# Performance work log

Measured on AMD Instinct MI355X. Metric: run time of the kernel, lower is better.

Reference implementation:

```python
import jax, jax.numpy as jnp
import numpy as np

D_MODEL = 1024
N_HEADS = 16
D_K = 64


def setup_inputs() -> dict:
    key = jax.random.key(0)
    ks = jax.random.split(key, 9)
    dkh = D_K * N_HEADS
    s = 1.0 / np.sqrt(D_MODEL)
    so = 1.0 / np.sqrt(dkh)
    return {
        "x": jax.random.normal(ks[0], (2, 2048, D_MODEL), dtype=jnp.float32),
        "Wq": jax.random.normal(ks[1], (D_MODEL, dkh), dtype=jnp.float32) * s,
        "bq": jnp.zeros((dkh,), dtype=jnp.float32),
        "Wk": jax.random.normal(ks[2], (D_MODEL, dkh), dtype=jnp.float32) * s,
        "bk": jnp.zeros((dkh,), dtype=jnp.float32),
        "Wv": jax.random.normal(ks[3], (D_MODEL, dkh), dtype=jnp.float32) * s,
        "bv": jnp.zeros((dkh,), dtype=jnp.float32),
        "Wo": jax.random.normal(ks[4], (dkh, D_MODEL), dtype=jnp.float32) * so,
        "bo": jnp.zeros((D_MODEL,), dtype=jnp.float32),
    }


def reference(x, Wq, bq, Wk, bk, Wv, bv, Wo, bo):
    B, S, _ = x.shape
    # project and split heads: [B, S, H, Dk] -> [B, H, S, Dk]
    def split(t):
        return t.reshape(B, S, N_HEADS, D_K).transpose(0, 2, 1, 3)
    q = split(x @ Wq + bq)
    k = split(x @ Wk + bk)
    v = split(x @ Wv + bv)
    scores = jnp.einsum("bhsd,bhtd->bhst", q, k) / jnp.sqrt(jnp.float32(D_K))
    weights = jax.nn.softmax(scores, axis=-1)
    out = jnp.einsum("bhst,bhtd->bhsd", weights, v)  # [B, H, S, Dk]
    out = out.transpose(0, 2, 1, 3).reshape(B, S, N_HEADS * D_K)
    return out @ Wo + bo
```

## Files before the change

kernel.cpp:

```cpp
#include <hip/hip_runtime.h>
#include <hip/hip_bf16.h>

typedef unsigned short u16;
typedef unsigned int u32;
typedef short bf16x4 __attribute__((ext_vector_type(4)));
typedef short bf16x8 __attribute__((ext_vector_type(8)));
typedef float f32x4 __attribute__((ext_vector_type(4)));
typedef u32 u32x2 __attribute__((ext_vector_type(2)));
typedef u32 u32x4 __attribute__((ext_vector_type(4)));

#define DEVINL __device__ __forceinline__

DEVINL u16 f2bf(float f) {
    u32 u = __builtin_bit_cast(u32, f);
    u32 r = u + 0x7fffu + ((u >> 16) & 1u);
    return (u16)(r >> 16);
}

DEVINL u32 pack2(float a, float b) {
    u16 lo = __builtin_bit_cast(u16, __float2bfloat16(a));
    u16 hi = __builtin_bit_cast(u16, __float2bfloat16(b));
    return (u32)lo | ((u32)hi << 16);
}

__global__ __launch_bounds__(256) void cast_x_kernel(const float4* __restrict__ in,
                                                     u16* __restrict__ outp) {
    int i = blockIdx.x * 256 + threadIdx.x;
    float4 v = in[i];
    ushort4 o;
    o.x = f2bf(v.x); o.y = f2bf(v.y); o.z = f2bf(v.z); o.w = f2bf(v.w);
    *(ushort4*)&outp[(size_t)i * 4] = o;
}

__global__ __launch_bounds__(256) void transpose_cast(
    const float* __restrict__ W0, const float* __restrict__ W1,
    const float* __restrict__ W2, const float* __restrict__ W3,
    u16* __restrict__ T0, u16* __restrict__ T1,
    u16* __restrict__ T2, u16* __restrict__ T3) {
    __shared__ __align__(16) u16 lds[64 * 68];
    int bid = blockIdx.x;
    const float* W; u16* T;
    switch (bid >> 8) {
        case 0:  W = W0; T = T0; break;
        case 1:  W = W1; T = T1; break;
        case 2:  W = W2; T = T2; break;
        default: W = W3; T = T3; break;
    }
    int tile = bid & 255;
    int k0 = (tile >> 4) << 6;
    int n0 = (tile & 15) << 6;
    int t = threadIdx.x;
    int rk = t >> 2;
    int cb = (t & 3) << 4;
#pragma unroll
    for (int j = 0; j < 4; ++j) {
        float4 v = *(const float4*)&W[(size_t)(k0 + rk) * 1024 + n0 + cb + 4 * j];
        ushort4 o;
        o.x = f2bf(v.x); o.y = f2bf(v.y); o.z = f2bf(v.z); o.w = f2bf(v.w);
        *(ushort4*)&lds[rk * 68 + cb + 4 * j] = o;
    }
    __syncthreads();
    int rn = t >> 2;
#pragma unroll
    for (int j2 = 0; j2 < 2; ++j2) {
        u16 tmp[8];
#pragma unroll
        for (int u = 0; u < 8; ++u)
            tmp[u] = lds[(cb + 8 * j2 + u) * 68 + rn];
        *(uint4*)&T[(size_t)(n0 + rn) * 1024 + k0 + cb + 8 * j2] = *(uint4*)tmp;
    }
}

template <int MODE>
__global__ __launch_bounds__(256) void gemm_kernel(
    const u16* __restrict__ A,
    const u16* __restrict__ W0t, const u16* __restrict__ W1t, const u16* __restrict__ W2t,
    const float* __restrict__ b0, const float* __restrict__ b1, const float* __restrict__ b2,
    u16* __restrict__ Oq, u16* __restrict__ Ok, u16* __restrict__ Ov,
    float* __restrict__ Fout) {
    constexpr int NB = (MODE == 0) ? 24 : 8;
    const int mb = blockIdx.x / NB, nb = blockIdx.x % NB;
    const int m0 = mb * 128, n0 = nb * 128;
    const int tid = threadIdx.x, lane = tid & 63, w = tid >> 6;
    const int wr = w >> 1, wc = w & 1;
    const int c = lane & 15, g = lane >> 4;

    __shared__ __align__(16) u16 Alds[128 * 64];
    __shared__ __align__(16) u16 Blds[128 * 64];

    const u16* Wt; const float* bias; int ncol0;
    if (MODE == 0) {
        const int tsel = n0 >> 10;
        Wt   = (tsel == 0) ? W0t : ((tsel == 1) ? W1t : W2t);
        bias = (tsel == 0) ? b0  : ((tsel == 1) ? b1  : b2);
        ncol0 = n0 & 1023;
    } else {
        Wt = W0t; bias = b0; ncol0 = n0;
    }

    const u16* Asrc = A  + (size_t)(m0    + 32 * w + (lane >> 3)) * 1024 + (lane & 7) * 8;
    const u16* Bsrc = Wt + (size_t)(ncol0 + 32 * w + (lane >> 3)) * 1024 + (lane & 7) * 8;
    u16* AldsW = &Alds[(32 * w) * 64];
    u16* BldsW = &Blds[(32 * w) * 64];

    f32x4 acc[4][4] = {};

    for (int kt = 0; kt < 16; ++kt) {
        const int k0 = kt * 64;
#pragma unroll
        for (int i = 0; i < 4; ++i) {
            __builtin_amdgcn_global_load_lds(
                (const __attribute__((address_space(1))) void*)(Asrc + k0 + i * 8 * 1024),
                (__attribute__((address_space(3))) void*)(AldsW + i * 8 * 64), 16, 0, 0);
            __builtin_amdgcn_global_load_lds(
                (const __attribute__((address_space(1))) void*)(Bsrc + k0 + i * 8 * 1024),
                (__attribute__((address_space(3))) void*)(BldsW + i * 8 * 64), 16, 0, 0);
        }
        __syncthreads();
#pragma unroll
        for (int kk = 0; kk < 2; ++kk) {
            bf16x8 af[4], bfr[4];
#pragma unroll
            for (int mf = 0; mf < 4; ++mf)
                af[mf] = *(const bf16x8*)&Alds[(c + 16 * mf + 64 * wr) * 64 + 8 * g + 32 * kk];
#pragma unroll
            for (int nf = 0; nf < 4; ++nf)
                bfr[nf] = *(const bf16x8*)&Blds[(c + 16 * nf + 64 * wc) * 64 + 8 * g + 32 * kk];
#pragma unroll
            for (int mf = 0; mf < 4; ++mf)
#pragma unroll
                for (int nf = 0; nf < 4; ++nf)
                    acc[mf][nf] = __builtin_amdgcn_mfma_f32_16x16x32_bf16(
                        af[mf], bfr[nf], acc[mf][nf], 0, 0, 0);
        }
        __syncthreads();
    }

    float biasv[4];
#pragma unroll
    for (int nf = 0; nf < 4; ++nf) biasv[nf] = bias[ncol0 + 64 * wc + 16 * nf + c];

    if (MODE == 0) {
        const int bi = m0 >> 11;
        const int tsel = n0 >> 10;
        if (tsel < 2) {
            u16* Odst = (tsel == 0) ? Oq : Ok;
            const float sc = (tsel == 0) ? 0.18033688011112042f : 1.0f;
#pragma unroll
            for (int nf = 0; nf < 4; ++nf) {
                const int n_in = ncol0 + 64 * wc + 16 * nf + c;
                const int h = n_in >> 6, d = n_in & 63;
                u16* base = Odst + ((size_t)(bi * 16 + h)) * 2048 * 64 + d;
#pragma unroll
                for (int mf = 0; mf < 4; ++mf)
#pragma unroll
                    for (int r = 0; r < 4; ++r) {
                        const int m = m0 + 64 * wr + 16 * mf + 4 * g + r;
                        const int s = m & 2047;
                        base[(size_t)s * 64] = f2bf((acc[mf][nf][r] + biasv[nf]) * sc);
                    }
            }
        } else {
#pragma unroll
            for (int nf = 0; nf < 4; ++nf) {
                const int n_in = ncol0 + 64 * wc + 16 * nf + c;
                const int h = n_in >> 6, d = n_in & 63;
                u16* base = Ov + ((size_t)((bi * 16 + h) * 64 + d)) * 2048;
#pragma unroll
                for (int mf = 0; mf < 4; ++mf) {
                    const int s = (m0 & 2047) + 64 * wr + 16 * mf + 4 * g;
                    const int r5 = s & 31;
                    const int pos = (s & ~63) + 32 * ((s >> 5) & 1)
                                  + ((r5 < 16) ? (2 * r5) : (2 * (r5 - 16) + 4));
                    u32x2 pr = {pack2(acc[mf][nf][0] + biasv[nf], acc[mf][nf][1] + biasv[nf]),
                                pack2(acc[mf][nf][2] + biasv[nf], acc[mf][nf][3] + biasv[nf])};
                    *(u32x2*)&base[pos] = pr;
                }
            }
        }
    } else {
#pragma unroll
        for (int mf = 0; mf < 4; ++mf)
#pragma unroll
            for (int r = 0; r < 4; ++r) {
                const int m = m0 + 64 * wr + 16 * mf + 4 * g + r;
                float* rowp = Fout + (size_t)m * 1024 + n0 + 64 * wc;
#pragma unroll
                for (int nf = 0; nf < 4; ++nf)
                    rowp[16 * nf + c] = acc[mf][nf][r] + biasv[nf];
            }
    }
}

__global__ __launch_bounds__(256) void attn_kernel(
    const u16* __restrict__ Q, const u16* __restrict__ K, const u16* __restrict__ Vp,
    u16* __restrict__ O) {
    const int bid0 = blockIdx.x;
    const int bid = (bid0 & 7) * 128 + (bid0 >> 3);
    const int qb = bid & 31, h = (bid >> 5) & 15, b = bid >> 9;
    const int tid = threadIdx.x, lane = tid & 63, w = tid >> 6;
    const int c = lane & 15, g = lane >> 4;

    __shared__ __align__(16) u16 KL[2][4096];
    __shared__ __align__(16) u16 VL[2][4096];

    const size_t hoff = ((size_t)(b * 16 + h)) * 2048 * 64;
    const u16* Qh = Q + hoff;
    const u16* Kh = K + hoff;
    const u16* Vh = Vp + hoff;

    const int q = qb * 64 + w * 16 + c;
    bf16x8 qf[2];
#pragma unroll
    for (int kk = 0; kk < 2; ++kk)
        qf[kk] = *(const bf16x8*)&Qh[(size_t)q * 64 + 8 * g + 32 * kk];

    const u16* kSrc = Kh + (size_t)(16 * w + (lane >> 2)) * 64 + 8 * (lane & 3);
    const u16* vSrc = Vh + (size_t)(16 * w + (lane >> 2)) * 2048 + 8 * (lane & 3);
    const int kdBase = (2 * w) * 512;

#define STAGE(bi_, kt_) do {                                                              \
        const u16* ks_ = kSrc + (kt_) * 4096;                                             \
        const u16* vs_ = vSrc + (kt_) * 64;                                               \
        __builtin_amdgcn_global_load_lds(                                                 \
            (const __attribute__((address_space(1))) void*)(ks_),                         \
            (__attribute__((address_space(3))) void*)(&KL[bi_][kdBase]), 16, 0, 0);       \
        __builtin_amdgcn_global_load_lds(                                                 \
            (const __attribute__((address_space(1))) void*)(ks_ + 32),                    \
            (__attribute__((address_space(3))) void*)(&KL[bi_][kdBase + 512]), 16, 0, 0); \
        __builtin_amdgcn_global_load_lds(                                                 \
            (const __attribute__((address_space(1))) void*)(vs_),                         \
            (__attribute__((address_space(3))) void*)(&VL[bi_][kdBase]), 16, 0, 0);       \
        __builtin_amdgcn_global_load_lds(                                                 \
            (const __attribute__((address_space(1))) void*)(vs_ + 32),                    \
            (__attribute__((address_space(3))) void*)(&VL[bi_][kdBase + 512]), 16, 0, 0); \
    } while (0)

    f32x4 oacc[4] = {};
    float mrun = -3.0e38f, lrun = 0.f;

    STAGE(0, 0);
    __syncthreads();

    for (int kt = 0; kt < 32; ++kt) {
        const int cur = kt & 1, nxt = cur ^ 1;
        if (kt < 31) STAGE(nxt, kt + 1);

        const u16* Kb0 = &KL[cur][0];
        const u16* Vb0 = &VL[cur][0];

        f32x4 sacc[4] = {};
#pragma unroll
        for (int T = 0; T < 4; ++T)
#pragma unroll
            for (int kk = 0; kk < 2; ++kk) {
                bf16x8 kf = *(const bf16x8*)&Kb0[(2 * T + kk) * 512 + 32 * c + 8 * g];
                sacc[T] = __builtin_amdgcn_mfma_f32_16x16x32_bf16(kf, qf[kk], sacc[T], 0, 0, 0);
            }

        float t0 = fmaxf(fmaxf(sacc[0][0], sacc[0][1]), fmaxf(sacc[0][2], sacc[0][3]));
        float t1 = fmaxf(fmaxf(sacc[1][0], sacc[1][1]), fmaxf(sacc[1][2], sacc[1][3]));
        float t2 = fmaxf(fmaxf(sacc[2][0], sacc[2][1]), fmaxf(sacc[2][2], sacc[2][3]));
        float t3 = fmaxf(fmaxf(sacc[3][0], sacc[3][1]), fmaxf(sacc[3][2], sacc[3][3]));
        float mx = fmaxf(fmaxf(t0, t1), fmaxf(t2, t3));
        mx = fmaxf(mx, __shfl_xor(mx, 16));
        mx = fmaxf(mx, __shfl_xor(mx, 32));

        if (__any(mx > mrun)) {
            const float mnew = fmaxf(mrun, mx);
            const float alpha = exp2f(mrun - mnew);
            mrun = mnew;
            lrun *= alpha;
#pragma unroll
            for (int dt = 0; dt < 4; ++dt)
#pragma unroll
                for (int r = 0; r < 4; ++r) oacc[dt][r] *= alpha;
        }

        u32 pw[4][2];
        float lsum = 0.f;
#pragma unroll
        for (int T = 0; T < 4; ++T) {
            float p0 = exp2f(sacc[T][0] - mrun);
            float p1 = exp2f(sacc[T][1] - mrun);
            float p2 = exp2f(sacc[T][2] - mrun);
            float p3 = exp2f(sacc[T][3] - mrun);
            lsum += (p0 + p1) + (p2 + p3);
            pw[T][0] = pack2(p0, p1);
            pw[T][1] = pack2(p2, p3);
        }
        lsum += __shfl_xor(lsum, 16);
        lsum += __shfl_xor(lsum, 32);
        lrun += lsum;

#pragma unroll
        for (int kb = 0; kb < 2; ++kb) {
            u32x4 ww = {pw[2 * kb][0], pw[2 * kb][1], pw[2 * kb + 1][0], pw[2 * kb + 1][1]};
            bf16x8 pf = __builtin_bit_cast(bf16x8, ww);
#pragma unroll
            for (int dt = 0; dt < 4; ++dt) {
                bf16x8 vf = *(const bf16x8*)&Vb0[(2 * dt + kb) * 512 + 32 * c + 8 * g];
                oacc[dt] = __builtin_amdgcn_mfma_f32_16x16x32_bf16(vf, pf, oacc[dt], 0, 0, 0);
            }
        }

        __syncthreads();
    }
#undef STAGE

    const float inv = 1.0f / lrun;
    const size_t obase = ((size_t)(b * 2048 + q)) * 1024 + h * 64 + 4 * g;
#pragma unroll
    for (int dt = 0; dt < 4; ++dt) {
        u32x2 pr = {pack2(oacc[dt][0] * inv, oacc[dt][1] * inv),
                    pack2(oacc[dt][2] * inv, oacc[dt][3] * inv)};
        *(u32x2*)&O[obase + 16 * dt] = pr;
    }
}

extern "C" void kernel_launch(void* const* d_in, const int* in_sizes, int n_in,
                              void* d_out, int out_size, void* d_ws, size_t ws_size,
                              hipStream_t stream) {
    const float* x  = (const float*)d_in[0];
    const float* Wq = (const float*)d_in[1];
    const float* bq = (const float*)d_in[2];
    const float* Wk = (const float*)d_in[3];
    const float* bk = (const float*)d_in[4];
    const float* Wv = (const float*)d_in[5];
    const float* bv = (const float*)d_in[6];
    const float* Wo = (const float*)d_in[7];
    const float* bo = (const float*)d_in[8];
    float* out = (float*)d_out;

    if (ws_size < (size_t)51 * 1024 * 1024) return;

    u16* ws  = (u16*)d_ws;
    u16* xb  = ws;
    u16* wqt = xb  + 4096 * 1024;
    u16* wkt = wqt + 1024 * 1024;
    u16* wvt = wkt + 1024 * 1024;
    u16* wot = wvt + 1024 * 1024;
    u16* Qb  = wot + 1024 * 1024;
    u16* Kb  = Qb + 4194304;
    u16* Vtb = Kb + 4194304;
    u16* Ob  = Vtb + 4194304;

    cast_x_kernel<<<4096, 256, 0, stream>>>((const float4*)x, xb);
    transpose_cast<<<1024, 256, 0, stream>>>(Wq, Wk, Wv, Wo, wqt, wkt, wvt, wot);
    gemm_kernel<0><<<768, 256, 0, stream>>>(xb, wqt, wkt, wvt, bq, bk, bv,
                                            Qb, Kb, Vtb, nullptr);
    attn_kernel<<<1024, 256, 0, stream>>>(Qb, Kb, Vtb, Ob);
    gemm_kernel<1><<<256, 256, 0, stream>>>(Ob, wot, nullptr, nullptr, bo, nullptr, nullptr,
                                            nullptr, nullptr, nullptr, out);
}
```

Measured before the change: 252.0 us.

## Enlarge attention query tile to 256 rows with 8 waves, two row tiles each

The attention kernel now uses 512-thread blocks covering 256 query rows, with each wave handling two 16-row query tiles that share every K/V fragment read from LDS. Each staged K/V tile is therefore reused by four times as many queries, which cuts global and LDS traffic per query, and the load work is spread across 8 waves. The softmax exponent switches from exp2f to __expf, and the Q prescale changes from 1/sqrt(64)*log2(e) to 1/8 so the two stay consistent. In exchange the grid shrinks to 256 blocks, roughly one per CU, and register pressure rises from the doubled accumulators, which may lower occupancy.

```diff
diff --git a/kernel.cpp b/kernel.cpp
--- a/kernel.cpp
+++ b/kernel.cpp
@@ -145,7 +145,7 @@
         const int tsel = n0 >> 10;
         if (tsel < 2) {
             u16* Odst = (tsel == 0) ? Oq : Ok;
-            const float sc = (tsel == 0) ? 0.18033688011112042f : 1.0f;
+            const float sc = (tsel == 0) ? 0.125f : 1.0f;
 #pragma unroll
             for (int nf = 0; nf < 4; ++nf) {
                 const int n_in = ncol0 + 64 * wc + 16 * nf + c;
@@ -192,12 +192,12 @@
     }
 }
 
-__global__ __launch_bounds__(256) void attn_kernel(
+__global__ __launch_bounds__(512) void attn_kernel(
     const u16* __restrict__ Q, const u16* __restrict__ K, const u16* __restrict__ Vp,
     u16* __restrict__ O) {
     const int bid0 = blockIdx.x;
-    const int bid = (bid0 & 7) * 128 + (bid0 >> 3);
-    const int qb = bid & 31, h = (bid >> 5) & 15, b = bid >> 9;
+    const int bid = (bid0 & 7) * 32 + (bid0 >> 3);
+    const int qb = bid & 7, h = (bid >> 3) & 15, b = bid >> 7;
     const int tid = threadIdx.x, lane = tid & 63, w = tid >> 6;
     const int c = lane & 15, g = lane >> 4;
 
@@ -209,35 +209,29 @@
     const u16* Kh = K + hoff;
     const u16* Vh = Vp + hoff;
 
-    const int q = qb * 64 + w * 16 + c;
-    bf16x8 qf[2];
-#pragma unroll
-    for (int kk = 0; kk < 2; ++kk)
-        qf[kk] = *(const bf16x8*)&Qh[(size_t)q * 64 + 8 * g + 32 * kk];
-
-    const u16* kSrc = Kh + (size_t)(16 * w + (lane >> 2)) * 64 + 8 * (lane & 3);
-    const u16* vSrc = Vh + (size_t)(16 * w + (lane >> 2)) * 2048 + 8 * (lane & 3);
-    const int kdBase = (2 * w) * 512;
+    const int q0 = qb * 256 + w * 32;
+    bf16x8 qf[2][2];
+#pragma unroll
+    for (int u = 0; u < 2; ++u)
+#pragma unroll
+        for (int kk = 0; kk < 2; ++kk)
+            qf[u][kk] = *(const bf16x8*)&Qh[(size_t)(q0 + 16 * u + c) * 64 + 8 * g + 32 * kk];
+
+    const u16* kSrc = Kh + (size_t)(16 * (w >> 1) + (lane >> 2)) * 64 + 32 * (w & 1) + 8 * (lane & 3);
+    const u16* vSrc = Vh + (size_t)(16 * (w >> 1) + (lane >> 2)) * 2048 + 32 * (w & 1) + 8 * (lane & 3);
+    const int dBase = w * 512;
 
 #define STAGE(bi_, kt_) do {                                                              \
-        const u16* ks_ = kSrc + (kt_) * 4096;                                             \
-        const u16* vs_ = vSrc + (kt_) * 64;                                               \
         __builtin_amdgcn_global_load_lds(                                                 \
-            (const __attribute__((address_space(1))) void*)(ks_),                         \
-            (__attribute__((address_space(3))) void*)(&KL[bi_][kdBase]), 16, 0, 0);       \
+            (const __attribute__((address_space(1))) void*)(kSrc + (kt_) * 4096),         \
+            (__attribute__((address_space(3))) void*)(&KL[bi_][dBase]), 16, 0, 0);        \
         __builtin_amdgcn_global_load_lds(                                                 \
-            (const __attribute__((address_space(1))) void*)(ks_ + 32),                    \
-            (__attribute__((address_space(3))) void*)(&KL[bi_][kdBase + 512]), 16, 0, 0); \
-        __builtin_amdgcn_global_load_lds(                                                 \
-            (const __attribute__((address_space(1))) void*)(vs_),                         \
-            (__attribute__((address_space(3))) void*)(&VL[bi_][kdBase]), 16, 0, 0);       \
-        __builtin_amdgcn_global_load_lds(                                                 \
-            (const __attribute__((address_space(1))) void*)(vs_ + 32),                    \
-            (__attribute__((address_space(3))) void*)(&VL[bi_][kdBase + 512]), 16, 0, 0); \
+            (const __attribute__((address_space(1))) void*)(vSrc + (kt_) * 64),           \
+            (__attribute__((address_space(3))) void*)(&VL[bi_][dBase]), 16, 0, 0);        \
     } while (0)
 
-    f32x4 oacc[4] = {};
-    float mrun = -3.0e38f, lrun = 0.f;
+    f32x4 oacc[2][4] = {};
+    float mrun[2] = {-3.0e38f, -3.0e38f}, lrun[2] = {0.f, 0.f};
 
     STAGE(0, 0);
     __syncthreads();
@@ -249,58 +243,65 @@
         const u16* Kb0 = &KL[cur][0];
         const u16* Vb0 = &VL[cur][0];
 
-        f32x4 sacc[4] = {};
+        f32x4 sacc[2][4] = {};
 #pragma unroll
         for (int T = 0; T < 4; ++T)
 #pragma unroll
             for (int kk = 0; kk < 2; ++kk) {
                 bf16x8 kf = *(const bf16x8*)&Kb0[(2 * T + kk) * 512 + 32 * c + 8 * g];
-                sacc[T] = __builtin_amdgcn_mfma_f32_16x16x32_bf16(kf, qf[kk], sacc[T], 0, 0, 0);
-            }
-
-        float t0 = fmaxf(fmaxf(sacc[0][0], sacc[0][1]), fmaxf(sacc[0][2], sacc[0][3]));
-        float t1 = fmaxf(fmaxf(sacc[1][0], sacc[1][1]), fmaxf(sacc[1][2], sacc[1][3]));
-        float t2 = fmaxf(fmaxf(sacc[2][0], sacc[2][1]), fmaxf(sacc[2][2], sacc[2][3]));
-        float t3 = fmaxf(fmaxf(sacc[3][0], sacc[3][1]), fmaxf(sacc[3][2], sacc[3][3]));
-        float mx = fmaxf(fmaxf(t0, t1), fmaxf(t2, t3));
-        mx = fmaxf(mx, __shfl_xor(mx, 16));
-        mx = fmaxf(mx, __shfl_xor(mx, 32));
-
-        if (__any(mx > mrun)) {
-            const float mnew = fmaxf(mrun, mx);
-            const float alpha = exp2f(mrun - mnew);
-            mrun = mnew;
-            lrun *= alpha;
-#pragma unroll
-            for (int dt = 0; dt < 4; ++dt)
-#pragma unroll
-                for (int r = 0; r < 4; ++r) oacc[dt][r] *= alpha;
-        }
-
-        u32 pw[4][2];
-        float lsum = 0.f;
-#pragma unroll
-        for (int T = 0; T < 4; ++T) {
-            float p0 = exp2f(sacc[T][0] - mrun);
-            float p1 = exp2f(sacc[T][1] - mrun);
-            float p2 = exp2f(sacc[T][2] - mrun);
-            float p3 = exp2f(sacc[T][3] - mrun);
-            lsum += (p0 + p1) + (p2 + p3);
-            pw[T][0] = pack2(p0, p1);
-            pw[T][1] = pack2(p2, p3);
-        }
-        lsum += __shfl_xor(lsum, 16);
-        lsum += __shfl_xor(lsum, 32);
-        lrun += lsum;
+                sacc[0][T] = __builtin_amdgcn_mfma_f32_16x16x32_bf16(kf, qf[0][kk], sacc[0][T], 0, 0, 0);
+                sacc[1][T] = __builtin_amdgcn_mfma_f32_16x16x32_bf16(kf, qf[1][kk], sacc[1][T], 0, 0, 0);
+            }
+
+        u32 pw[2][4][2];
+#pragma unroll
+        for (int u = 0; u < 2; ++u) {
+            float t0 = fmaxf(fmaxf(sacc[u][0][0], sacc[u][0][1]), fmaxf(sacc[u][0][2], sacc[u][0][3]));
+            float t1 = fmaxf(fmaxf(sacc[u][1][0], sacc[u][1][1]), fmaxf(sacc[u][1][2], sacc[u][1][3]));
+            float t2 = fmaxf(fmaxf(sacc[u][2][0], sacc[u][2][1]), fmaxf(sacc[u][2][2], sacc[u][2][3]));
+            float t3 = fmaxf(fmaxf(sacc[u][3][0], sacc[u][3][1]), fmaxf(sacc[u][3][2], sacc[u][3][3]));
+            float mx = fmaxf(fmaxf(t0, t1), fmaxf(t2, t3));
+            mx = fmaxf(mx, __shfl_xor(mx, 16));
+            mx = fmaxf(mx, __shfl_xor(mx, 32));
+
+            if (__any(mx > mrun[u])) {
+                const float mnew = fmaxf(mrun[u], mx);
+                const float alpha = __expf(mrun[u] - mnew);
+                mrun[u] = mnew;
+                lrun[u] *= alpha;
+#pragma unroll
+                for (int dt = 0; dt < 4; ++dt)
+#pragma unroll
+                    for (int r = 0; r < 4; ++r) oacc[u][dt][r] *= alpha;
+            }
+
+            float lsum = 0.f;
+#pragma unroll
+            for (int T = 0; T < 4; ++T) {
+                float p0 = __expf(sacc[u][T][0] - mrun[u]);
+                float p1 = __expf(sacc[u][T][1] - mrun[u]);
+                float p2 = __expf(sacc[u][T][2] - mrun[u]);
+                float p3 = __expf(sacc[u][T][3] - mrun[u]);
+                lsum += (p0 + p1) + (p2 + p3);
+                pw[u][T][0] = pack2(p0, p1);
+                pw[u][T][1] = pack2(p2, p3);
+            }
+            lsum += __shfl_xor(lsum, 16);
+            lsum += __shfl_xor(lsum, 32);
+            lrun[u] += lsum;
+        }
 
 #pragma unroll
         for (int kb = 0; kb < 2; ++kb) {
-            u32x4 ww = {pw[2 * kb][0], pw[2 * kb][1], pw[2 * kb + 1][0], pw[2 * kb + 1][1]};
-            bf16x8 pf = __builtin_bit_cast(bf16x8, ww);
+            u32x4 w0 = {pw[0][2 * kb][0], pw[0][2 * kb][1], pw[0][2 * kb + 1][0], pw[0][2 * kb + 1][1]};
+            u32x4 w1 = {pw[1][2 * kb][0], pw[1][2 * kb][1], pw[1][2 * kb + 1][0], pw[1][2 * kb + 1][1]};
+            bf16x8 pf0 = __builtin_bit_cast(bf16x8, w0);
+            bf16x8 pf1 = __builtin_bit_cast(bf16x8, w1);
 #pragma unroll
             for (int dt = 0; dt < 4; ++dt) {
                 bf16x8 vf = *(const bf16x8*)&Vb0[(2 * dt + kb) * 512 + 32 * c + 8 * g];
-                oacc[dt] = __builtin_amdgcn_mfma_f32_16x16x32_bf16(vf, pf, oacc[dt], 0, 0, 0);
+                oacc[0][dt] = __builtin_amdgcn_mfma_f32_16x16x32_bf16(vf, pf0, oacc[0][dt], 0, 0, 0);
+                oacc[1][dt] = __builtin_amdgcn_mfma_f32_16x16x32_bf16(vf, pf1, oacc[1][dt], 0, 0, 0);
             }
         }
 
@@ -308,13 +309,16 @@
     }
 #undef STAGE
 
-    const float inv = 1.0f / lrun;
-    const size_t obase = ((size_t)(b * 2048 + q)) * 1024 + h * 64 + 4 * g;
-#pragma unroll
-    for (int dt = 0; dt < 4; ++dt) {
-        u32x2 pr = {pack2(oacc[dt][0] * inv, oacc[dt][1] * inv),
-                    pack2(oacc[dt][2] * inv, oacc[dt][3] * inv)};
-        *(u32x2*)&O[obase + 16 * dt] = pr;
+#pragma unroll
+    for (int u = 0; u < 2; ++u) {
+        const float inv = 1.0f / lrun[u];
+        const size_t obase = ((size_t)(b * 2048 + q0 + 16 * u + c)) * 1024 + h * 64 + 4 * g;
+#pragma unroll
+        for (int dt = 0; dt < 4; ++dt) {
+            u32x2 pr = {pack2(oacc[u][dt][0] * inv, oacc[u][dt][1] * inv),
+                        pack2(oacc[u][dt][2] * inv, oacc[u][dt][3] * inv)};
+            *(u32x2*)&O[obase + 16 * dt] = pr;
+        }
     }
 }
 
@@ -349,7 +353,7 @@
     transpose_cast<<<1024, 256, 0, stream>>>(Wq, Wk, Wv, Wo, wqt, wkt, wvt, wot);
     gemm_kernel<0><<<768, 256, 0, stream>>>(xb, wqt, wkt, wvt, bq, bk, bv,
                                             Qb, Kb, Vtb, nullptr);
-    attn_kernel<<<1024, 256, 0, stream>>>(Qb, Kb, Vtb, Ob);
+    attn_kernel<<<256, 512, 0, stream>>>(Qb, Kb, Vtb, Ob);
     gemm_kernel<1><<<256, 256, 0, stream>>>(Ob, wot, nullptr, nullptr, bo, nullptr, nullptr,
                                             nullptr, nullptr, nullptr, out);
 }
```

New measurement: 232.4 us. -7.8%, faster.
